# Kernel optimization log

Hardware: AMD Instinct MI355X
Metric: run time of the kernel (lower is better)

## Reference

```python
import jax, jax.numpy as jnp
import numpy as np

B, S, D_MODEL, H, D_HEAD = 4, 2048, 1024, 16, 64
SCALE = D_HEAD ** -0.5


def setup_inputs() -> dict:
    key = jax.random.key(0)
    ks = jax.random.split(key, 6)
    init = lambda k, shp: jax.random.normal(k, shp, jnp.float32) * (shp[0] ** -0.5)
    Xq = jax.random.normal(ks[0], (B, S, D_MODEL), jnp.float32)
    # pre-softmax bool mask: True = masked (fill -inf) -> causal
    mask_bef = jnp.triu(jnp.ones((S, S), dtype=bool), k=1)
    # post-softmax bool mask: True = zero out that attention weight
    mask_aft = jax.random.bernoulli(ks[1], 0.1, (S, S))
    Wq = init(ks[2], (D_MODEL, H * D_HEAD))
    Wk = init(ks[3], (D_MODEL, H * D_HEAD))
    Wv = init(ks[4], (D_MODEL, H * D_HEAD))
    Wo = init(ks[5], (H * D_HEAD, D_MODEL))
    return {"Xq": Xq, "mask_bef": mask_bef, "mask_aft": mask_aft,
            "Wq": Wq, "Wk": Wk, "Wv": Wv, "Wo": Wo}


def reference(Xq, mask_bef, mask_aft, Wq, Wk, Wv, Wo):
    # Self-attention: Xk = Xv = Xq
    def split_heads(X, W):  # [B,S,D] @ [D,H*d] -> [B,H,S,d]
        return (X @ W).reshape(B, S, H, D_HEAD).transpose(0, 2, 1, 3)

    Q = split_heads(Xq, Wq)
    K = split_heads(Xq, Wk)
    V = split_heads(Xq, Wv)
    # scores: [B,H,Sq,Sk]
    scores = jnp.einsum('bhqd,bhkd->bhqk', Q, K) * SCALE
    scores = jnp.where(mask_bef, -jnp.inf, scores)  # pre-softmax bool mask
    attn = jax.nn.softmax(scores, axis=-1)
    attn = jnp.where(mask_aft, 0.0, attn)           # post-softmax bool mask
    out = jnp.einsum('bhqk,bhkd->bhqd', attn, V)    # [B,H,S,d]
    out = out.transpose(0, 2, 1, 3).reshape(B, S, H * D_HEAD)
    return out @ Wo  # [B,S,out_dim_o]
```

## Files before the change

### kernel.cpp

```cpp
#include <hip/hip_runtime.h>
#include <hip/hip_bf16.h>


using bf16 = __hip_bfloat16;
typedef __attribute__((ext_vector_type(8))) short short8;
typedef __attribute__((ext_vector_type(4))) float floatx4;

#define kB 4
#define kS 2048
#define kDM 1024
#define kH 16
#define kDH 64
#define kHeadElems ((size_t)kB * kH * kS * kDH)
#define STR 72

#if __has_builtin(__builtin_amdgcn_exp2f)
#define EXP2(x) __builtin_amdgcn_exp2f(x)
#else
#define EXP2(x) __expf((x) * 0.69314718056f)
#endif

__device__ __forceinline__ unsigned short f2bf(float f) {
    union { float f; unsigned u; } x{f};
    unsigned r = x.u + 0x7fff + ((x.u >> 16) & 1);
    return (unsigned short)(r >> 16);
}
__device__ __forceinline__ void gl_lds16(const void* g, void* l) {
    __builtin_amdgcn_global_load_lds(
        (const __attribute__((address_space(1))) unsigned int*)g,
        (__attribute__((address_space(3))) unsigned int*)l, 16, 0, 0);
}

__global__ __launch_bounds__(256)
void pack_em(const int* __restrict__ mask_aft, unsigned short* __restrict__ EM)
{
    const size_t i = ((size_t)blockIdx.x * 256 + threadIdx.x) * 8;
    const int q  = (int)(i >> 11);
    const int k0 = (int)(i & 2047);
    const int4 m0 = *(const int4*)(mask_aft + i);
    const int4 m1 = *(const int4*)(mask_aft + i + 4);
    union { unsigned short u[8]; uint4 v; } o;
    o.u[0] = (m0.x || (k0 + 0) > q) ? 0 : 0xFFFFu;
    o.u[1] = (m0.y || (k0 + 1) > q) ? 0 : 0xFFFFu;
    o.u[2] = (m0.z || (k0 + 2) > q) ? 0 : 0xFFFFu;
    o.u[3] = (m0.w || (k0 + 3) > q) ? 0 : 0xFFFFu;
    o.u[4] = (m1.x || (k0 + 4) > q) ? 0 : 0xFFFFu;
    o.u[5] = (m1.y || (k0 + 5) > q) ? 0 : 0xFFFFu;
    o.u[6] = (m1.z || (k0 + 6) > q) ? 0 : 0xFFFFu;
    o.u[7] = (m1.w || (k0 + 7) > q) ? 0 : 0xFFFFu;
    *(uint4*)(EM + i) = o.v;
}

__global__ __launch_bounds__(256)
void conv_x(const float* __restrict__ X, bf16* __restrict__ Xb)
{
    const size_t i = ((size_t)blockIdx.x * 256 + threadIdx.x) * 8;
    const float4 a = *(const float4*)(X + i);
    const float4 b = *(const float4*)(X + i + 4);
    union { unsigned short u[8]; uint4 v; } o;
    o.u[0] = f2bf(a.x); o.u[1] = f2bf(a.y); o.u[2] = f2bf(a.z); o.u[3] = f2bf(a.w);
    o.u[4] = f2bf(b.x); o.u[5] = f2bf(b.y); o.u[6] = f2bf(b.z); o.u[7] = f2bf(b.w);
    *(uint4*)(Xb + i) = o.v;
}

__global__ __launch_bounds__(256)
void conv_wT(const float* __restrict__ W, bf16* __restrict__ WT)
{
    __shared__ unsigned short Ls[64][STR];
    const int k0 = blockIdx.x * 64, n0 = blockIdx.y * 64;
    const int tid = threadIdx.x;
    const int r16 = tid >> 4, c4 = (tid & 15) * 4;
    #pragma unroll
    for (int it = 0; it < 4; ++it) {
        const int r = it * 16 + r16;
        const float4 v = *(const float4*)(W + (size_t)(k0 + r) * kDM + n0 + c4);
        Ls[c4 + 0][r] = f2bf(v.x); Ls[c4 + 1][r] = f2bf(v.y);
        Ls[c4 + 2][r] = f2bf(v.z); Ls[c4 + 3][r] = f2bf(v.w);
    }
    __syncthreads();
    #pragma unroll
    for (int it = 0; it < 4; ++it) {
        const int rn = it * 16 + r16;
        ushort4 u;
        u.x = Ls[rn][c4 + 0]; u.y = Ls[rn][c4 + 1];
        u.z = Ls[rn][c4 + 2]; u.w = Ls[rn][c4 + 3];
        *(ushort4*)(WT + (size_t)(n0 + rn) * kDM + k0 + c4) = u;
    }
}

__global__ __launch_bounds__(256)
void qkv_mfma(const bf16* __restrict__ A, const bf16* __restrict__ BT,
              bf16* __restrict__ ws)
{
    __shared__ __align__(16) unsigned short At[128][32];
    __shared__ __align__(16) unsigned short Bt[128][32];
    const int tid = threadIdx.x;
    const int w = tid >> 6, lane = tid & 63;
    const int quad = (tid >> 4) & 3, col = tid & 15;
    const int wm = w >> 1, wn = w & 1;
    const int n0 = blockIdx.x * 128;
    const int m0 = blockIdx.y * 128;

    const bf16* pA = A  + (size_t)(m0 + w * 32 + (lane >> 2)) * kDM + (lane & 3) * 8;
    const bf16* pB = BT + (size_t)(n0 + w * 32 + (lane >> 2)) * kDM + (lane & 3) * 8;
    unsigned short* lA = &At[w * 32][0];
    unsigned short* lB = &Bt[w * 32][0];

    floatx4 acc[4][4];
    #pragma unroll
    for (int i = 0; i < 4; ++i)
        #pragma unroll
        for (int j = 0; j < 4; ++j) acc[i][j] = (floatx4){0.f, 0.f, 0.f, 0.f};

    for (int k0 = 0; k0 < kDM; k0 += 32) {
        __syncthreads();
        gl_lds16(pA + k0, lA);
        gl_lds16(pA + k0 + 16 * kDM, lA + 16 * 32);
        gl_lds16(pB + k0, lB);
        gl_lds16(pB + k0 + 16 * kDM, lB + 16 * 32);
        __syncthreads();
        short8 aA[4], bB[4];
        #pragma unroll
        for (int i = 0; i < 4; ++i)
            aA[i] = *(const short8*)&At[wm * 64 + i * 16 + col][quad * 8];
        #pragma unroll
        for (int j = 0; j < 4; ++j)
            bB[j] = *(const short8*)&Bt[wn * 64 + j * 16 + col][quad * 8];
        #pragma unroll
        for (int i = 0; i < 4; ++i)
            #pragma unroll
            for (int j = 0; j < 4; ++j)
                acc[i][j] = __builtin_amdgcn_mfma_f32_16x16x32_bf16(aA[i], bB[j], acc[i][j], 0, 0, 0);
    }

    const int p  = n0 >> 10;
    const int nn = n0 & 1023;
    const float scl = (p == 0) ? 0.18033688f : 1.0f;
    bf16* Out = ws + (size_t)p * kHeadElems;
    #pragma unroll
    for (int i = 0; i < 4; ++i) {
        #pragma unroll
        for (int r = 0; r < 4; ++r) {
            const int m = m0 + wm * 64 + i * 16 + quad * 4 + r;
            const int b = m >> 11, s = m & 2047;
            #pragma unroll
            for (int j = 0; j < 4; ++j) {
                const int n = nn + wn * 64 + j * 16 + col;
                const int h = n >> 6, d = n & 63;
                Out[((size_t)(b * kH + h) * kS + s) * kDH + d] = __float2bfloat16(acc[i][j][r] * scl);
            }
        }
    }
}

__global__ __launch_bounds__(256)
void vtrans(const bf16* __restrict__ V, bf16* __restrict__ VT)
{
    const int bh = blockIdx.y;
    const int s0 = blockIdx.x * 64;
    const bf16* src = V + (size_t)bh * kS * kDH;
    bf16* dst = VT + (size_t)bh * kS * kDH;
    __shared__ unsigned short L[64][STR];
    const int tid = threadIdx.x;
    #pragma unroll
    for (int t = 0; t < 2; ++t) {
        const int idx = t * 256 + tid;
        const int r = idx >> 3, c8 = (idx & 7) * 8;
        *(uint4*)&L[r][c8] = *(const uint4*)(src + (size_t)(s0 + r) * kDH + c8);
    }
    __syncthreads();
    #pragma unroll
    for (int t = 0; t < 2; ++t) {
        const int idx = t * 256 + tid;
        const int d = idx >> 3, sc = (idx & 7) * 8;
        unsigned short tmp[8];
        #pragma unroll
        for (int e = 0; e < 8; ++e) tmp[e] = L[sc + e][d];
        *(uint4*)(dst + (size_t)d * kS + s0 + sc) = *(uint4*)tmp;
    }
}

__global__ __launch_bounds__(256, 3)
void attn_mfma(const bf16* __restrict__ ws, const bf16* __restrict__ VT,
               const unsigned short* __restrict__ EM,
               bf16* __restrict__ Aout)
{
    const int flat = blockIdx.x + blockIdx.y * 16;
    const int xcd = flat & 7;
    const int idx = flat >> 3;
    const int bh  = xcd * 8 + (idx & 7);
    const int j   = idx >> 3;
    const int qtile = (j & 1) ? (j >> 1) : (15 - (j >> 1));
    const int q0 = qtile * 128;

    const int b = bh >> 4, h = bh & 15;
    const int tid  = threadIdx.x;
    const int w    = tid >> 6;
    const int lane = tid & 63;
    const int quad = (tid >> 4) & 3;
    const int col  = tid & 15;

    const size_t ho = (size_t)bh * kS * kDH;
    const bf16* Qg  = ws + ho;
    const bf16* Kg  = ws + kHeadElems + ho;
    const bf16* VTg = VT + ho;

    __shared__ __align__(16) unsigned short Ks[2][64][64];
    __shared__ __align__(16) unsigned short Vs[2][64][64];
    __shared__ __align__(16) unsigned short Pw[4][2][16][STR];

    const int qw = q0 + w * 32;
    const int swz = col & 7;
    const int sch = (lane & 7) ^ (lane >> 3);

    short8 bQ[2][2];
    const unsigned short* EMq[2];
    #pragma unroll
    for (int sub = 0; sub < 2; ++sub) {
        const bf16* qrow = Qg + (size_t)(qw + sub * 16 + col) * kDH;
        bQ[sub][0] = *(const short8*)(qrow + quad * 8);
        bQ[sub][1] = *(const short8*)(qrow + 32 + quad * 8);
        EMq[sub] = EM + (size_t)(qw + sub * 16 + col) * kS;
    }

    floatx4 Ov[2][4];
    #pragma unroll
    for (int sub = 0; sub < 2; ++sub)
        #pragma unroll
        for (int dg = 0; dg < 4; ++dg) Ov[sub][dg] = (floatx4){0.f, 0.f, 0.f, 0.f};
    float lacc[2] = {0.f, 0.f};

    const int nt = qtile * 2 + 2;

    auto STAGE = [&](int buf, int kt) {
        const bf16* Kt = Kg  + (size_t)(kt * 64) * kDH;
        const bf16* Vt = VTg + kt * 64;
        #pragma unroll
        for (int t = 0; t < 2; ++t) {
            const int rbase = (t * 4 + w) * 8;
            const int r = rbase + (lane >> 3);
            gl_lds16(Kt + (size_t)r * kDH + sch * 8, &Ks[buf][rbase][0]);
            gl_lds16(Vt + (size_t)r * kS  + sch * 8, &Vs[buf][rbase][0]);
        }
    };

    STAGE(0, 0);
    asm volatile("s_waitcnt vmcnt(0)" ::: "memory");
    __builtin_amdgcn_s_barrier();
    __builtin_amdgcn_sched_barrier(0);

    int cur = 0;
    for (int kt = 0; kt < nt; ++kt) {
        if (kt + 1 < nt) STAGE(cur ^ 1, kt + 1);

        const int kt64 = kt * 64;
        if (kt64 <= qw + 31) {
            floatx4 sg[2][4];
            __builtin_amdgcn_s_setprio(1);
            #pragma unroll
            for (int g = 0; g < 4; ++g) {
                const int krow = g * 16 + col;
                const short8 aK0 = *(const short8*)&Ks[cur][krow][(quad ^ swz) * 8];
                const short8 aK1 = *(const short8*)&Ks[cur][krow][((4 + quad) ^ swz) * 8];
                floatx4 sA = {0.f, 0.f, 0.f, 0.f}, sB = {0.f, 0.f, 0.f, 0.f};
                sA = __builtin_amdgcn_mfma_f32_16x16x32_bf16(aK0, bQ[0][0], sA, 0, 0, 0);
                sA = __builtin_amdgcn_mfma_f32_16x16x32_bf16(aK1, bQ[0][1], sA, 0, 0, 0);
                sB = __builtin_amdgcn_mfma_f32_16x16x32_bf16(aK0, bQ[1][0], sB, 0, 0, 0);
                sB = __builtin_amdgcn_mfma_f32_16x16x32_bf16(aK1, bQ[1][1], sB, 0, 0, 0);
                sg[0][g] = sA; sg[1][g] = sB;
            }
            __builtin_amdgcn_s_setprio(0);

            #pragma unroll
            for (int sub = 0; sub < 2; ++sub) {
                const int qbase = qw + sub * 16;
                const bool needC = (kt64 + 63 > qbase);
                float lc = 0.f;
                #pragma unroll
                for (int g = 0; g < 4; ++g) {
                    const float p0 = EXP2(sg[sub][g][0]);
                    const float p1 = EXP2(sg[sub][g][1]);
                    const float p2 = EXP2(sg[sub][g][2]);
                    const float p3 = EXP2(sg[sub][g][3]);
                    if (needC) {
                        const int kb = kt64 + g * 16 + quad * 4;
                        const int qme = qbase + col;
                        lc += (kb + 0 <= qme) ? p0 : 0.f;
                        lc += (kb + 1 <= qme) ? p1 : 0.f;
                        lc += (kb + 2 <= qme) ? p2 : 0.f;
                        lc += (kb + 3 <= qme) ? p3 : 0.f;
                    } else {
                        lc += (p0 + p1) + (p2 + p3);
                    }
                    const unsigned b0 = __float_as_uint(p0) + 0x8000u;
                    const unsigned b1 = __float_as_uint(p1) + 0x8000u;
                    const unsigned b2 = __float_as_uint(p2) + 0x8000u;
                    const unsigned b3 = __float_as_uint(p3) + 0x8000u;
                    uint2 pk;
                    pk.x = __builtin_amdgcn_perm(b1, b0, 0x07060302u);
                    pk.y = __builtin_amdgcn_perm(b3, b2, 0x07060302u);
                    const uint2 em = *(const uint2*)(EMq[sub] + kt64 + g * 16 + quad * 4);
                    pk.x &= em.x; pk.y &= em.y;
                    *(uint2*)&Pw[w][sub][col][g * 16 + quad * 4] = pk;
                }
                lacc[sub] += lc;
            }

            const short8 aP[2][2] = {
                { *(const short8*)&Pw[w][0][col][quad * 8],
                  *(const short8*)&Pw[w][0][col][32 + quad * 8] },
                { *(const short8*)&Pw[w][1][col][quad * 8],
                  *(const short8*)&Pw[w][1][col][32 + quad * 8] } };
            __builtin_amdgcn_s_setprio(1);
            #pragma unroll
            for (int dg = 0; dg < 4; ++dg) {
                const int vrow = dg * 16 + col;
                const short8 bV0 = *(const short8*)&Vs[cur][vrow][(quad ^ swz) * 8];
                const short8 bV1 = *(const short8*)&Vs[cur][vrow][((4 + quad) ^ swz) * 8];
                Ov[0][dg] = __builtin_amdgcn_mfma_f32_16x16x32_bf16(aP[0][0], bV0, Ov[0][dg], 0, 0, 0);
                Ov[0][dg] = __builtin_amdgcn_mfma_f32_16x16x32_bf16(aP[0][1], bV1, Ov[0][dg], 0, 0, 0);
                Ov[1][dg] = __builtin_amdgcn_mfma_f32_16x16x32_bf16(aP[1][0], bV0, Ov[1][dg], 0, 0, 0);
                Ov[1][dg] = __builtin_amdgcn_mfma_f32_16x16x32_bf16(aP[1][1], bV1, Ov[1][dg], 0, 0, 0);
            }
            __builtin_amdgcn_s_setprio(0);
        }

        asm volatile("s_waitcnt vmcnt(0)" ::: "memory");
        __builtin_amdgcn_s_barrier();
        __builtin_amdgcn_sched_barrier(0);
        cur ^= 1;
    }

    #pragma unroll
    for (int sub = 0; sub < 2; ++sub) {
        float l = lacc[sub];
        l += __shfl_xor(l, 16, 64);
        l += __shfl_xor(l, 32, 64);
        const float linv = 1.f / l;
        #pragma unroll
        for (int r = 0; r < 4; ++r) {
            const float sc = __shfl(linv, quad * 4 + r, 64);
            const int q = qw + sub * 16 + quad * 4 + r;
            bf16* orow = Aout + ((size_t)(b * kS + q)) * kDM + h * kDH;
            #pragma unroll
            for (int dg = 0; dg < 4; ++dg)
                orow[dg * 16 + col] = __float2bfloat16(Ov[sub][dg][r] * sc);
        }
    }
}

__global__ __launch_bounds__(256)
void out_mfma(const bf16* __restrict__ A, const bf16* __restrict__ BT,
              float* __restrict__ Out)
{
    __shared__ __align__(16) unsigned short At[128][32];
    __shared__ __align__(16) unsigned short Bt[128][32];
    const int tid = threadIdx.x;
    const int w = tid >> 6, lane = tid & 63;
    const int quad = (tid >> 4) & 3, col = tid & 15;
    const int wm = w >> 1, wn = w & 1;
    const int n0 = blockIdx.x * 128;
    const int m0 = blockIdx.y * 128;

    const bf16* pA = A  + (size_t)(m0 + w * 32 + (lane >> 2)) * kDM + (lane & 3) * 8;
    const bf16* pB = BT + (size_t)(n0 + w * 32 + (lane >> 2)) * kDM + (lane & 3) * 8;
    unsigned short* lA = &At[w * 32][0];
    unsigned short* lB = &Bt[w * 32][0];

    floatx4 acc[4][4];
    #pragma unroll
    for (int i = 0; i < 4; ++i)
        #pragma unroll
        for (int j = 0; j < 4; ++j) acc[i][j] = (floatx4){0.f, 0.f, 0.f, 0.f};

    for (int k0 = 0; k0 < kDM; k0 += 32) {
        __syncthreads();
        gl_lds16(pA + k0, lA);
        gl_lds16(pA + k0 + 16 * kDM, lA + 16 * 32);
        gl_lds16(pB + k0, lB);
        gl_lds16(pB + k0 + 16 * kDM, lB + 16 * 32);
        __syncthreads();
        short8 aA[4], bB[4];
        #pragma unroll
        for (int i = 0; i < 4; ++i)
            aA[i] = *(const short8*)&At[wm * 64 + i * 16 + col][quad * 8];
        #pragma unroll
        for (int j = 0; j < 4; ++j)
            bB[j] = *(const short8*)&Bt[wn * 64 + j * 16 + col][quad * 8];
        #pragma unroll
        for (int i = 0; i < 4; ++i)
            #pragma unroll
            for (int j = 0; j < 4; ++j)
                acc[i][j] = __builtin_amdgcn_mfma_f32_16x16x32_bf16(aA[i], bB[j], acc[i][j], 0, 0, 0);
    }

    #pragma unroll
    for (int i = 0; i < 4; ++i)
        #pragma unroll
        for (int r = 0; r < 4; ++r) {
            const int m = m0 + wm * 64 + i * 16 + quad * 4 + r;
            #pragma unroll
            for (int j = 0; j < 4; ++j)
                Out[(size_t)m * kDM + n0 + wn * 64 + j * 16 + col] = acc[i][j][r];
        }
}

extern "C" void kernel_launch(void* const* d_in, const int* in_sizes, int n_in,
                              void* d_out, int out_size, void* d_ws, size_t ws_size,
                              hipStream_t stream)
{
    const float* Xq       = (const float*)d_in[0];
    const int*   mask_aft = (const int*)d_in[2];
    const float* Wq       = (const float*)d_in[3];
    const float* Wk       = (const float*)d_in[4];
    const float* Wv       = (const float*)d_in[5];
    const float* Wo       = (const float*)d_in[6];
    float* out = (float*)d_out;

    bf16* ws   = (bf16*)d_ws;
    bf16* Xbf  = ws + 3 * kHeadElems;
    bf16* Aout = Xbf;
    bf16* WoT  = ws;

    bf16* WcatT = (bf16*)d_out + 262144;
    bf16* VT    = (bf16*)((char*)d_out + 8u * 1024 * 1024);
    unsigned short* EMp = (unsigned short*)((char*)d_out + 24u * 1024 * 1024);

    pack_em <<<dim3(2048), 256, 0, stream>>>(mask_aft, EMp);
    conv_x  <<<dim3(4096), 256, 0, stream>>>(Xq, Xbf);
    conv_wT <<<dim3(16, 16), 256, 0, stream>>>(Wq, WcatT);
    conv_wT <<<dim3(16, 16), 256, 0, stream>>>(Wk, WcatT + (size_t)kDM * kDM);
    conv_wT <<<dim3(16, 16), 256, 0, stream>>>(Wv, WcatT + 2 * (size_t)kDM * kDM);
    qkv_mfma<<<dim3(24, 64), 256, 0, stream>>>(Xbf, WcatT, ws);
    vtrans  <<<dim3(32, 64), 256, 0, stream>>>(ws + 2 * kHeadElems, VT);
    attn_mfma<<<dim3(16, 64), 256, 0, stream>>>(ws, VT, EMp, Aout);
    conv_wT <<<dim3(16, 16), 256, 0, stream>>>(Wo, WoT);
    out_mfma<<<dim3(8, 64), 256, 0, stream>>>(Aout, WoT, out);
}
```

Measured before the change: 340.2 us.

## Triple-buffer K/V tiles with prefetch distance two and hoist mask loads

Replaces the double-buffered K/V staging with a three-deep ring so loads run two tiles ahead, using partial vmcnt waits instead of draining all loads every iteration. The post-softmax mask loads for a tile are issued before the staging loads, so they can complete during the QK MFMAs. The causal q-tile ordering across blocks is also changed for load balance, and launch bounds are lowered to two blocks per CU to fit the extra LDS and registers. The cost is reduced occupancy and more shared memory per block.

```diff
diff --git a/kernel.cpp b/kernel.cpp
--- a/kernel.cpp
+++ b/kernel.cpp
@@ -180,7 +180,7 @@
     }
 }
 
-__global__ __launch_bounds__(256, 3)
+__global__ __launch_bounds__(256, 2)
 void attn_mfma(const bf16* __restrict__ ws, const bf16* __restrict__ VT,
                const unsigned short* __restrict__ EM,
                bf16* __restrict__ Aout)
@@ -190,7 +190,8 @@
     const int idx = flat >> 3;
     const int bh  = xcd * 8 + (idx & 7);
     const int j   = idx >> 3;
-    const int qtile = (j & 1) ? (j >> 1) : (15 - (j >> 1));
+    const int kk  = 3 - (j >> 2);
+    const int qtile = 4 * kk + ((kk + (j & 3)) & 3);
     const int q0 = qtile * 128;
 
     const int b = bh >> 4, h = bh & 15;
@@ -205,8 +206,8 @@
     const bf16* Kg  = ws + kHeadElems + ho;
     const bf16* VTg = VT + ho;
 
-    __shared__ __align__(16) unsigned short Ks[2][64][64];
-    __shared__ __align__(16) unsigned short Vs[2][64][64];
+    __shared__ __align__(16) unsigned short Ks[3][64][64];
+    __shared__ __align__(16) unsigned short Vs[3][64][64];
     __shared__ __align__(16) unsigned short Pw[4][2][16][STR];
 
     const int qw = q0 + w * 32;
@@ -245,16 +246,29 @@
     };
 
     STAGE(0, 0);
-    asm volatile("s_waitcnt vmcnt(0)" ::: "memory");
+    STAGE(1, 1);
+    asm volatile("s_waitcnt vmcnt(4)" ::: "memory");
     __builtin_amdgcn_s_barrier();
     __builtin_amdgcn_sched_barrier(0);
 
-    int cur = 0;
+    int cur = 0, stg = 2;
     for (int kt = 0; kt < nt; ++kt) {
-        if (kt + 1 < nt) STAGE(cur ^ 1, kt + 1);
-
         const int kt64 = kt * 64;
-        if (kt64 <= qw + 31) {
+        const bool doC = (kt64 <= qw + 31);
+
+        uint2 em[2][4];
+        if (doC) {
+            #pragma unroll
+            for (int sub = 0; sub < 2; ++sub)
+                #pragma unroll
+                for (int g = 0; g < 4; ++g)
+                    em[sub][g] = *(const uint2*)(EMq[sub] + kt64 + g * 16 + quad * 4);
+            __builtin_amdgcn_sched_barrier(0);
+        }
+
+        if (kt + 2 < nt) STAGE(stg, kt + 2);
+
+        if (doC) {
             floatx4 sg[2][4];
             __builtin_amdgcn_s_setprio(1);
             #pragma unroll
@@ -299,8 +313,7 @@
                     uint2 pk;
                     pk.x = __builtin_amdgcn_perm(b1, b0, 0x07060302u);
                     pk.y = __builtin_amdgcn_perm(b3, b2, 0x07060302u);
-                    const uint2 em = *(const uint2*)(EMq[sub] + kt64 + g * 16 + quad * 4);
-                    pk.x &= em.x; pk.y &= em.y;
+                    pk.x &= em[sub][g].x; pk.y &= em[sub][g].y;
                     *(uint2*)&Pw[w][sub][col][g * 16 + quad * 4] = pk;
                 }
                 lacc[sub] += lc;
@@ -325,10 +338,15 @@
             __builtin_amdgcn_s_setprio(0);
         }
 
-        asm volatile("s_waitcnt vmcnt(0)" ::: "memory");
+        if (kt + 2 < nt) {
+            asm volatile("s_waitcnt vmcnt(4)" ::: "memory");
+        } else {
+            asm volatile("s_waitcnt vmcnt(0)" ::: "memory");
+        }
         __builtin_amdgcn_s_barrier();
         __builtin_amdgcn_sched_barrier(0);
-        cur ^= 1;
+        cur = (cur == 2) ? 0 : cur + 1;
+        stg = (stg == 2) ? 0 : stg + 1;
     }
 
     #pragma unroll
```

After: 326.7 us. 4.0% less time.

## Enlarge attention query tile to 256 rows and remap GEMM block order for XCD locality

Applied to the files above, without the earlier changes.

The attention kernel now processes 256 query rows per block with four 16-row sub-tiles per wave, interleaved across waves, so each staged K/V tile is reused by twice as many queries. Global K/V traffic and barrier overhead per query drop, at the cost of more accumulator registers, which lowers occupancy (launch bounds 3 to 2) and halves the grid. It also prefetches mask words into registers before the loop body, converts P to bf16 with a packed v_cvt_pk_bf16_f32 instruction, and remaps block indices in the QKV and output GEMMs to group tiles per XCD for better L2 reuse.

```diff
diff --git a/kernel.cpp b/kernel.cpp
--- a/kernel.cpp
+++ b/kernel.cpp
@@ -24,6 +24,11 @@
     union { float f; unsigned u; } x{f};
     unsigned r = x.u + 0x7fff + ((x.u >> 16) & 1);
     return (unsigned short)(r >> 16);
+}
+__device__ __forceinline__ unsigned cvt_pk_bf16(float lo, float hi) {
+    unsigned r;
+    asm("v_cvt_pk_bf16_f32 %0, %1, %2" : "=v"(r) : "v"(lo), "v"(hi));
+    return r;
 }
 __device__ __forceinline__ void gl_lds16(const void* g, void* l) {
     __builtin_amdgcn_global_load_lds(
@@ -98,8 +103,11 @@
     const int w = tid >> 6, lane = tid & 63;
     const int quad = (tid >> 4) & 3, col = tid & 15;
     const int wm = w >> 1, wn = w & 1;
-    const int n0 = blockIdx.x * 128;
-    const int m0 = blockIdx.y * 128;
+    const int flat = blockIdx.x + blockIdx.y * 24;
+    const int xcd = flat & 7;
+    const int i2 = flat >> 3;
+    const int n0 = (xcd * 3 + (i2 % 3)) * 128;
+    const int m0 = (i2 / 3) * 128;
 
     const bf16* pA = A  + (size_t)(m0 + w * 32 + (lane >> 2)) * kDM + (lane & 3) * 8;
     const bf16* pB = BT + (size_t)(n0 + w * 32 + (lane >> 2)) * kDM + (lane & 3) * 8;
@@ -180,18 +188,18 @@
     }
 }
 
-__global__ __launch_bounds__(256, 3)
+__global__ __launch_bounds__(256, 2)
 void attn_mfma(const bf16* __restrict__ ws, const bf16* __restrict__ VT,
                const unsigned short* __restrict__ EM,
                bf16* __restrict__ Aout)
 {
-    const int flat = blockIdx.x + blockIdx.y * 16;
+    const int flat = blockIdx.x + blockIdx.y * 8;
     const int xcd = flat & 7;
     const int idx = flat >> 3;
     const int bh  = xcd * 8 + (idx & 7);
     const int j   = idx >> 3;
-    const int qtile = (j & 1) ? (j >> 1) : (15 - (j >> 1));
-    const int q0 = qtile * 128;
+    const int tq  = (j < 4) ? (7 - j) : (j - 4);
+    const int q0 = tq * 256;
 
     const int b = bh >> 4, h = bh & 15;
     const int tid  = threadIdx.x;
@@ -207,30 +215,30 @@
 
     __shared__ __align__(16) unsigned short Ks[2][64][64];
     __shared__ __align__(16) unsigned short Vs[2][64][64];
-    __shared__ __align__(16) unsigned short Pw[4][2][16][STR];
-
-    const int qw = q0 + w * 32;
+    __shared__ __align__(16) unsigned short Pw[4][16][STR];
+
     const int swz = col & 7;
     const int sch = (lane & 7) ^ (lane >> 3);
 
-    short8 bQ[2][2];
-    const unsigned short* EMq[2];
-    #pragma unroll
-    for (int sub = 0; sub < 2; ++sub) {
-        const bf16* qrow = Qg + (size_t)(qw + sub * 16 + col) * kDH;
+    short8 bQ[4][2];
+    const unsigned short* EMq[4];
+    #pragma unroll
+    for (int sub = 0; sub < 4; ++sub) {
+        const int qr = q0 + sub * 64 + w * 16;
+        const bf16* qrow = Qg + (size_t)(qr + col) * kDH;
         bQ[sub][0] = *(const short8*)(qrow + quad * 8);
         bQ[sub][1] = *(const short8*)(qrow + 32 + quad * 8);
-        EMq[sub] = EM + (size_t)(qw + sub * 16 + col) * kS;
-    }
-
-    floatx4 Ov[2][4];
-    #pragma unroll
-    for (int sub = 0; sub < 2; ++sub)
+        EMq[sub] = EM + (size_t)(qr + col) * kS;
+    }
+
+    floatx4 Ov[4][4];
+    #pragma unroll
+    for (int sub = 0; sub < 4; ++sub)
         #pragma unroll
         for (int dg = 0; dg < 4; ++dg) Ov[sub][dg] = (floatx4){0.f, 0.f, 0.f, 0.f};
-    float lacc[2] = {0.f, 0.f};
-
-    const int nt = qtile * 2 + 2;
+    float lacc[4] = {0.f, 0.f, 0.f, 0.f};
+
+    const int nt = tq * 4 + 4;
 
     auto STAGE = [&](int buf, int kt) {
         const bf16* Kt = Kg  + (size_t)(kt * 64) * kDH;
@@ -251,37 +259,50 @@
 
     int cur = 0;
     for (int kt = 0; kt < nt; ++kt) {
+        const int kt64 = kt * 64;
+
+        uint2 em[4][4];
+        #pragma unroll
+        for (int sub = 0; sub < 4; ++sub)
+            #pragma unroll
+            for (int g = 0; g < 4; ++g)
+                em[sub][g] = *(const uint2*)(EMq[sub] + kt64 + g * 16 + quad * 4);
+        __builtin_amdgcn_sched_barrier(0);
+
         if (kt + 1 < nt) STAGE(cur ^ 1, kt + 1);
 
-        const int kt64 = kt * 64;
-        if (kt64 <= qw + 31) {
-            floatx4 sg[2][4];
-            __builtin_amdgcn_s_setprio(1);
-            #pragma unroll
-            for (int g = 0; g < 4; ++g) {
-                const int krow = g * 16 + col;
-                const short8 aK0 = *(const short8*)&Ks[cur][krow][(quad ^ swz) * 8];
-                const short8 aK1 = *(const short8*)&Ks[cur][krow][((4 + quad) ^ swz) * 8];
-                floatx4 sA = {0.f, 0.f, 0.f, 0.f}, sB = {0.f, 0.f, 0.f, 0.f};
-                sA = __builtin_amdgcn_mfma_f32_16x16x32_bf16(aK0, bQ[0][0], sA, 0, 0, 0);
-                sA = __builtin_amdgcn_mfma_f32_16x16x32_bf16(aK1, bQ[0][1], sA, 0, 0, 0);
-                sB = __builtin_amdgcn_mfma_f32_16x16x32_bf16(aK0, bQ[1][0], sB, 0, 0, 0);
-                sB = __builtin_amdgcn_mfma_f32_16x16x32_bf16(aK1, bQ[1][1], sB, 0, 0, 0);
-                sg[0][g] = sA; sg[1][g] = sB;
-            }
-            __builtin_amdgcn_s_setprio(0);
-
-            #pragma unroll
-            for (int sub = 0; sub < 2; ++sub) {
-                const int qbase = qw + sub * 16;
+        short8 aK[4][2];
+        #pragma unroll
+        for (int g = 0; g < 4; ++g) {
+            const int krow = g * 16 + col;
+            aK[g][0] = *(const short8*)&Ks[cur][krow][(quad ^ swz) * 8];
+            aK[g][1] = *(const short8*)&Ks[cur][krow][((4 + quad) ^ swz) * 8];
+        }
+
+        short8 aP[4][2];
+        #pragma unroll
+        for (int sub = 0; sub < 4; ++sub) {
+            const int qbase = q0 + sub * 64 + w * 16;
+            if (kt64 <= qbase + 15) {
+                floatx4 sg[4];
+                __builtin_amdgcn_s_setprio(1);
+                #pragma unroll
+                for (int g = 0; g < 4; ++g) {
+                    floatx4 s = {0.f, 0.f, 0.f, 0.f};
+                    s = __builtin_amdgcn_mfma_f32_16x16x32_bf16(aK[g][0], bQ[sub][0], s, 0, 0, 0);
+                    s = __builtin_amdgcn_mfma_f32_16x16x32_bf16(aK[g][1], bQ[sub][1], s, 0, 0, 0);
+                    sg[g] = s;
+                }
+                __builtin_amdgcn_s_setprio(0);
+
                 const bool needC = (kt64 + 63 > qbase);
                 float lc = 0.f;
                 #pragma unroll
                 for (int g = 0; g < 4; ++g) {
-                    const float p0 = EXP2(sg[sub][g][0]);
-                    const float p1 = EXP2(sg[sub][g][1]);
-                    const float p2 = EXP2(sg[sub][g][2]);
-                    const float p3 = EXP2(sg[sub][g][3]);
+                    const float p0 = EXP2(sg[g][0]);
+                    const float p1 = EXP2(sg[g][1]);
+                    const float p2 = EXP2(sg[g][2]);
+                    const float p3 = EXP2(sg[g][3]);
                     if (needC) {
                         const int kb = kt64 + g * 16 + quad * 4;
                         const int qme = qbase + col;
@@ -292,38 +313,33 @@
                     } else {
                         lc += (p0 + p1) + (p2 + p3);
                     }
-                    const unsigned b0 = __float_as_uint(p0) + 0x8000u;
-                    const unsigned b1 = __float_as_uint(p1) + 0x8000u;
-                    const unsigned b2 = __float_as_uint(p2) + 0x8000u;
-                    const unsigned b3 = __float_as_uint(p3) + 0x8000u;
                     uint2 pk;
-                    pk.x = __builtin_amdgcn_perm(b1, b0, 0x07060302u);
-                    pk.y = __builtin_amdgcn_perm(b3, b2, 0x07060302u);
-                    const uint2 em = *(const uint2*)(EMq[sub] + kt64 + g * 16 + quad * 4);
-                    pk.x &= em.x; pk.y &= em.y;
-                    *(uint2*)&Pw[w][sub][col][g * 16 + quad * 4] = pk;
+                    pk.x = cvt_pk_bf16(p0, p1) & em[sub][g].x;
+                    pk.y = cvt_pk_bf16(p2, p3) & em[sub][g].y;
+                    *(uint2*)&Pw[w][col][g * 16 + quad * 4] = pk;
                 }
                 lacc[sub] += lc;
+                aP[sub][0] = *(const short8*)&Pw[w][col][quad * 8];
+                aP[sub][1] = *(const short8*)&Pw[w][col][32 + quad * 8];
             }
-
-            const short8 aP[2][2] = {
-                { *(const short8*)&Pw[w][0][col][quad * 8],
-                  *(const short8*)&Pw[w][0][col][32 + quad * 8] },
-                { *(const short8*)&Pw[w][1][col][quad * 8],
-                  *(const short8*)&Pw[w][1][col][32 + quad * 8] } };
-            __builtin_amdgcn_s_setprio(1);
-            #pragma unroll
-            for (int dg = 0; dg < 4; ++dg) {
-                const int vrow = dg * 16 + col;
-                const short8 bV0 = *(const short8*)&Vs[cur][vrow][(quad ^ swz) * 8];
-                const short8 bV1 = *(const short8*)&Vs[cur][vrow][((4 + quad) ^ swz) * 8];
-                Ov[0][dg] = __builtin_amdgcn_mfma_f32_16x16x32_bf16(aP[0][0], bV0, Ov[0][dg], 0, 0, 0);
-                Ov[0][dg] = __builtin_amdgcn_mfma_f32_16x16x32_bf16(aP[0][1], bV1, Ov[0][dg], 0, 0, 0);
-                Ov[1][dg] = __builtin_amdgcn_mfma_f32_16x16x32_bf16(aP[1][0], bV0, Ov[1][dg], 0, 0, 0);
-                Ov[1][dg] = __builtin_amdgcn_mfma_f32_16x16x32_bf16(aP[1][1], bV1, Ov[1][dg], 0, 0, 0);
+        }
+
+        __builtin_amdgcn_s_setprio(1);
+        #pragma unroll
+        for (int dg = 0; dg < 4; ++dg) {
+            const int vrow = dg * 16 + col;
+            const short8 bV0 = *(const short8*)&Vs[cur][vrow][(quad ^ swz) * 8];
+            const short8 bV1 = *(const short8*)&Vs[cur][vrow][((4 + quad) ^ swz) * 8];
+            #pragma unroll
+            for (int sub = 0; sub < 4; ++sub) {
+                const int qbase = q0 + sub * 64 + w * 16;
+                if (kt64 <= qbase + 15) {
+                    Ov[sub][dg] = __builtin_amdgcn_mfma_f32_16x16x32_bf16(aP[sub][0], bV0, Ov[sub][dg], 0, 0, 0);
+                    Ov[sub][dg] = __builtin_amdgcn_mfma_f32_16x16x32_bf16(aP[sub][1], bV1, Ov[sub][dg], 0, 0, 0);
+                }
             }
-            __builtin_amdgcn_s_setprio(0);
-        }
+        }
+        __builtin_amdgcn_s_setprio(0);
 
         asm volatile("s_waitcnt vmcnt(0)" ::: "memory");
         __builtin_amdgcn_s_barrier();
@@ -332,15 +348,16 @@
     }
 
     #pragma unroll
-    for (int sub = 0; sub < 2; ++sub) {
+    for (int sub = 0; sub < 4; ++sub) {
         float l = lacc[sub];
         l += __shfl_xor(l, 16, 64);
         l += __shfl_xor(l, 32, 64);
         const float linv = 1.f / l;
+        const int qbase = q0 + sub * 64 + w * 16;
         #pragma unroll
         for (int r = 0; r < 4; ++r) {
             const float sc = __shfl(linv, quad * 4 + r, 64);
-            const int q = qw + sub * 16 + quad * 4 + r;
+            const int q = qbase + quad * 4 + r;
             bf16* orow = Aout + ((size_t)(b * kS + q)) * kDM + h * kDH;
             #pragma unroll
             for (int dg = 0; dg < 4; ++dg)
@@ -359,8 +376,9 @@
     const int w = tid >> 6, lane = tid & 63;
     const int quad = (tid >> 4) & 3, col = tid & 15;
     const int wm = w >> 1, wn = w & 1;
-    const int n0 = blockIdx.x * 128;
-    const int m0 = blockIdx.y * 128;
+    const int flat = blockIdx.x + blockIdx.y * 8;
+    const int n0 = (flat & 7) * 128;
+    const int m0 = (flat >> 3) * 128;
 
     const bf16* pA = A  + (size_t)(m0 + w * 32 + (lane >> 2)) * kDM + (lane & 3) * 8;
     const bf16* pB = BT + (size_t)(n0 + w * 32 + (lane >> 2)) * kDM + (lane & 3) * 8;
@@ -433,7 +451,7 @@
     conv_wT <<<dim3(16, 16), 256, 0, stream>>>(Wv, WcatT + 2 * (size_t)kDM * kDM);
     qkv_mfma<<<dim3(24, 64), 256, 0, stream>>>(Xbf, WcatT, ws);
     vtrans  <<<dim3(32, 64), 256, 0, stream>>>(ws + 2 * kHeadElems, VT);
-    attn_mfma<<<dim3(16, 64), 256, 0, stream>>>(ws, VT, EMp, Aout);
+    attn_mfma<<<dim3(8, 64), 256, 0, stream>>>(ws, VT, EMp, Aout);
     conv_wT <<<dim3(16, 16), 256, 0, stream>>>(Wo, WoT);
     out_mfma<<<dim3(8, 64), 256, 0, stream>>>(Aout, WoT, out);
 }
```

Result: slower. 358.2 us (+5.3%).
